# Kernel tuning notes

Hardware: AMD Instinct MI355X
Metric: run time of the kernel (lower is better)

## Reference

```python
import jax, jax.numpy as jnp
import numpy as np

BETA = 0.25  # VectorQuantizer commitment beta


def setup_inputs() -> dict:
    key = jax.random.key(0)
    k1, k2, k3, k4 = jax.random.split(key, 4)
    B, T, Zc, D, K = 8, 4096, 512, 256, 8192
    x = jax.random.normal(k1, (B, T, 1, Zc), dtype=jnp.float32)
    W = jax.random.normal(k2, (Zc, D), dtype=jnp.float32) / np.sqrt(Zc)
    b = jax.random.normal(k3, (D,), dtype=jnp.float32) * 0.01
    codebook = jax.random.normal(k4, (K, D), dtype=jnp.float32) / np.sqrt(D)
    return {"x": x, "W": W, "b": b, "codebook": codebook}


def reference(x, W, b, codebook):
    sg = jax.lax.stop_gradient
    # quant_conv: Linear(z_channels -> embed_dim) after squeezing dim 2
    h = jnp.einsum('btc,cd->btd', jnp.squeeze(x, 2), W) + b  # [B,T,D]
    B, T, D = h.shape
    flat = h.reshape(-1, D)  # [B*T, D]
    # squared L2 distances to codebook: ||z||^2 + ||e||^2 - 2 z.e
    d = (jnp.sum(flat * flat, axis=1, keepdims=True)
         + jnp.sum(codebook * codebook, axis=1)
         - 2.0 * flat @ codebook.T)  # [B*T, K]
    idx = jnp.argmin(d, axis=1)  # [B*T]
    zq = jnp.take(codebook, idx, axis=0).reshape(B, T, D)
    # codebook + commitment loss
    emb_loss = (BETA * jnp.mean((sg(zq) - h) ** 2)
                + jnp.mean((zq - sg(h)) ** 2))
    # straight-through estimator
    zq = h + sg(zq - h)
    quant = zq[..., None]  # [B,T,D,1], matching h.unsqueeze(-1) layout
    return quant, emb_loss
```

## Files before the change

kernel.cpp:

```cpp
#include <hip/hip_runtime.h>
#include <stdint.h>

#define M_TOT 32768
#define ZC 512
#define DD 256
#define KCODES 8192
#define NGRAN 512
#define MARGIN 0.15f
#define NBUCKET 256

typedef _Float16 half8   __attribute__((ext_vector_type(8)));
typedef _Float16 half2v  __attribute__((ext_vector_type(2)));
typedef float    float4v __attribute__((ext_vector_type(4)));
typedef float    float16v __attribute__((ext_vector_type(16)));

#define OFF_H     0ull
#define OFF_HT    33554432ull
#define OFF_CBT   50331648ull
#define OFF_HH    54525952ull
#define OFF_EE    54657024ull
#define OFF_LOSSP 54689792ull
#define OFF_SMIN  54691840ull
#define OFF_WTH   OFF_SMIN
#define OFF_WTL   (OFF_SMIN + 524288ull)

#define ASYNC_CP16(gp, lp)                                                     \
  __builtin_amdgcn_global_load_lds(                                            \
      (const __attribute__((address_space(1))) void*)(gp),                     \
      (__attribute__((address_space(3))) void*)(lp), 16, 0, 0)

__global__ __launch_bounds__(256) void k_prep_w(const float* __restrict__ W,
                                                _Float16* __restrict__ wt_hi,
                                                _Float16* __restrict__ wt_lo) {
    const int idx = blockIdx.x * 256 + threadIdx.x;
    const int n = idx & 255, k = idx >> 8;
    const float v = W[(size_t)k * DD + n];
    const _Float16 hi = (_Float16)v;
    const _Float16 lo = (_Float16)(v - (float)hi);
    const int off = (((n >> 5) * 64 + (k >> 3)) << 8) + ((n & 31) << 3) + (k & 7);
    wt_hi[off] = hi;
    wt_lo[off] = lo;
}

__global__ __launch_bounds__(256) void k_gemm1(const float* __restrict__ x,
                                               const _Float16* __restrict__ wt_hi,
                                               const _Float16* __restrict__ wt_lo,
                                               const float* __restrict__ b,
                                               float* __restrict__ h) {
    __shared__ _Float16 sH[64 * 64];
    __shared__ _Float16 sL[64 * 64];
    const int tid = threadIdx.x, lane = tid & 63, w = tid >> 6;
    const int wy = w >> 1, wx = w & 1;
    const int m0 = blockIdx.x * 64;

    float16v acc[4];
#pragma unroll
    for (int j = 0; j < 4; ++j) acc[j] = (float16v)(0.0f);

    for (int kb = 0; kb < ZC; kb += 64) {
        __syncthreads();
        {
            const int m = tid & 63;
            const int kp = tid >> 6;
#pragma unroll
            for (int i2 = 0; i2 < 2; ++i2) {
                const int kg = kp * 2 + i2;
                const float* src = x + (size_t)(m0 + m) * ZC + kb + kg * 8;
                float4v v0 = *(const float4v*)src;
                float4v v1 = *(const float4v*)(src + 4);
                half8 hi, lo;
                float vv[8] = {v0.x, v0.y, v0.z, v0.w, v1.x, v1.y, v1.z, v1.w};
#pragma unroll
                for (int j = 0; j < 8; ++j) {
                    hi[j] = (_Float16)vv[j];
                    lo[j] = (_Float16)(vv[j] - (float)hi[j]);
                }
                const int off = (((m >> 5) * 8 + kg) << 8) + ((m & 31) << 3);
                *(half8*)&sH[off] = hi;
                *(half8*)&sL[off] = lo;
            }
        }
        __syncthreads();
#pragma unroll
        for (int s = 0; s < 4; ++s) {
            const int S = (kb >> 4) + s;
            half8 ah = *(const half8*)&sH[((wy * 8 + 2 * s) << 8) + lane * 8];
            half8 al = *(const half8*)&sL[((wy * 8 + 2 * s) << 8) + lane * 8];
#pragma unroll
            for (int nf = 0; nf < 4; ++nf) {
                const int nblk = wx * 4 + nf;
                const size_t boff = ((size_t)(nblk * 64 + 2 * S) << 8) + lane * 8;
                half8 bh = *(const half8*)&wt_hi[boff];
                half8 bl = *(const half8*)&wt_lo[boff];
                acc[nf] = __builtin_amdgcn_mfma_f32_32x32x16_f16(ah, bh, acc[nf], 0, 0, 0);
                acc[nf] = __builtin_amdgcn_mfma_f32_32x32x16_f16(ah, bl, acc[nf], 0, 0, 0);
                acc[nf] = __builtin_amdgcn_mfma_f32_32x32x16_f16(al, bh, acc[nf], 0, 0, 0);
            }
        }
    }
#pragma unroll
    for (int nf = 0; nf < 4; ++nf) {
        const int col = wx * 128 + nf * 32 + (lane & 31);
        const float bias = b[col];
#pragma unroll
        for (int r = 0; r < 16; ++r) {
            const int row = m0 + wy * 32 + (r & 3) + 8 * (r >> 2) + 4 * (lane >> 5);
            h[(size_t)row * DD + col] = acc[nf][r] + bias;
        }
    }
}

__global__ __launch_bounds__(256) void k_prep_h(const float* __restrict__ h,
                                                _Float16* __restrict__ ht,
                                                float* __restrict__ hh) {
    const int lane = threadIdx.x & 63, w = threadIdx.x >> 6;
    const int row = blockIdx.x * 4 + w;
    float4v v = *(const float4v*)&h[(size_t)row * DD + lane * 4];
    half2v p0, p1;
    p0.x = (_Float16)v.x; p0.y = (_Float16)v.y;
    p1.x = (_Float16)v.z; p1.y = (_Float16)v.w;
    const size_t off = ((size_t)((row >> 5) * 32 + (lane >> 1)) << 8) +
                       ((row & 31) << 3) + ((lane & 1) << 2);
    *(half2v*)&ht[off] = p0;
    *(half2v*)&ht[off + 2] = p1;
    float s = v.x * v.x + v.y * v.y + v.z * v.z + v.w * v.w;
#pragma unroll
    for (int o = 32; o; o >>= 1) s += __shfl_down(s, o);
    if (lane == 0) hh[row] = s;
}

__global__ __launch_bounds__(256) void k_prep_cb(const float* __restrict__ cb,
                                                 _Float16* __restrict__ cbt,
                                                 float* __restrict__ ee,
                                                 float* __restrict__ loss_part) {
    if (blockIdx.x == 0) loss_part[threadIdx.x] = 0.0f;
    const int lane = threadIdx.x & 63, w = threadIdx.x >> 6;
    const int code = blockIdx.x * 4 + w;
    float4v v = *(const float4v*)&cb[(size_t)code * DD + lane * 4];
    half2v p0, p1;
    p0.x = (_Float16)v.x; p0.y = (_Float16)v.y;
    p1.x = (_Float16)v.z; p1.y = (_Float16)v.w;
    const size_t off = ((size_t)((code >> 5) * 32 + (lane >> 1)) << 8) +
                       ((code & 31) << 3) + ((lane & 1) << 2);
    *(half2v*)&cbt[off] = p0;
    *(half2v*)&cbt[off + 2] = p1;
    float s = v.x * v.x + v.y * v.y + v.z * v.z + v.w * v.w;
#pragma unroll
    for (int o = 32; o; o >>= 1) s += __shfl_down(s, o);
    if (lane == 0) ee[code] = s;
}

__global__ __launch_bounds__(256, 2) void k_dist(const _Float16* __restrict__ ht,
                                                 const _Float16* __restrict__ cbt,
                                                 const float* __restrict__ ee,
                                                 _Float16* __restrict__ smin) {
    __shared__ _Float16 sB[2][64 * 256];
    const int tid = threadIdx.x, lane = tid & 63, w = tid >> 6;
    const int lw = lane & 31, csel = lane >> 5;
    const int bx = blockIdx.x;
    const int by = blockIdx.y;

    half8 afr[2][16];
    const size_t lo = (size_t)lane * 8;
#pragma unroll
    for (int mi = 0; mi < 2; ++mi) {
        const _Float16* base = cbt + (size_t)(bx * 8 + w * 2 + mi) * 8192;
#pragma unroll
        for (int s = 0; s < 16; ++s)
            afr[mi][s] = *(const half8*)(base + s * 512 + lo);
    }
    half8 aext[2], bext;
#pragma unroll
    for (int j = 0; j < 8; ++j) bext[j] = (_Float16)0.f;
    if (csel == 0) bext[0] = (_Float16)(-0.5f);
#pragma unroll
    for (int mi = 0; mi < 2; ++mi) {
        const float e = ee[bx * 256 + w * 64 + mi * 32 + lw];
#pragma unroll
        for (int j = 0; j < 8; ++j) aext[mi][j] = (_Float16)0.f;
        if (csel == 0) aext[mi][0] = (_Float16)e;
    }

    const _Float16* hbase = ht + (size_t)by * 1024 * 256 + (size_t)w * 4096 + lane * 8;
#define STAGE_HS(buf, t)                                                       \
    do {                                                                       \
        const _Float16* g_ = hbase + (size_t)(t) * 16384;                      \
        char* l_ = (char*)&sB[(buf)][0] + w * 8192;                            \
        _Pragma("unroll")                                                      \
        for (int i_ = 0; i_ < 8; ++i_)                                         \
            ASYNC_CP16(g_ + i_ * 512, l_ + i_ * 1024);                         \
    } while (0)

#define LDB(sb_, nj_, s_)                                                      \
    (*(const half8*)&(sb_)[(size_t)((((nj_) * 32) + 2 * (s_) + csel) << 8) + lw * 8])

#define EPI(accA, accB, nj_)                                                   \
    do {                                                                       \
        float g0a = (accA)[0], g1a = (accA)[8];                                \
        float g0b = (accB)[0], g1b = (accB)[8];                                \
        _Pragma("unroll")                                                      \
        for (int r = 1; r < 8; ++r) {                                          \
            g0a = fmaxf(g0a, (accA)[r]);  g1a = fmaxf(g1a, (accA)[8 + r]);     \
            g0b = fmaxf(g0b, (accB)[r]);  g1b = fmaxf(g1b, (accB)[8 + r]);     \
        }                                                                      \
        g0a = fmaxf(g0a, __shfl_xor(g0a, 32));                                 \
        g1a = fmaxf(g1a, __shfl_xor(g1a, 32));                                 \
        g0b = fmaxf(g0b, __shfl_xor(g0b, 32));                                 \
        g1b = fmaxf(g1b, __shfl_xor(g1b, 32));                                 \
        if (lane < 32) {                                                       \
            const int row_ = r0_ + (nj_) * 32 + lane;                          \
            const int gb_ = bx * 16 + w * 4;                                   \
            smin[(size_t)(gb_ + 0) * M_TOT + row_] = (_Float16)(-2.f * g0a);   \
            smin[(size_t)(gb_ + 1) * M_TOT + row_] = (_Float16)(-2.f * g1a);   \
            smin[(size_t)(gb_ + 2) * M_TOT + row_] = (_Float16)(-2.f * g0b);   \
            smin[(size_t)(gb_ + 3) * M_TOT + row_] = (_Float16)(-2.f * g1b);   \
        }                                                                      \
    } while (0)

#define COMPUTE_HS(buf, t)                                                     \
    do {                                                                       \
        const int r0_ = by * 1024 + (t) * 64;                                  \
        const _Float16* sb_ = &sB[(buf)][0];                                   \
        float16v A00 = (float16v)(0.f), A01 = (float16v)(0.f);                 \
        float16v A10 = (float16v)(0.f), A11 = (float16v)(0.f);                 \
        __builtin_amdgcn_s_setprio(1);                                         \
        _Pragma("unroll")                                                      \
        for (int s = 0; s < 16; ++s) {                                         \
            half8 bf0 = LDB(sb_, 0, s);                                        \
            half8 bf1 = LDB(sb_, 1, s);                                        \
            A00 = __builtin_amdgcn_mfma_f32_32x32x16_f16(afr[0][s], bf0, A00, 0, 0, 0); \
            A01 = __builtin_amdgcn_mfma_f32_32x32x16_f16(afr[1][s], bf0, A01, 0, 0, 0); \
            A10 = __builtin_amdgcn_mfma_f32_32x32x16_f16(afr[0][s], bf1, A10, 0, 0, 0); \
            A11 = __builtin_amdgcn_mfma_f32_32x32x16_f16(afr[1][s], bf1, A11, 0, 0, 0); \
        }                                                                      \
        A00 = __builtin_amdgcn_mfma_f32_32x32x16_f16(aext[0], bext, A00, 0, 0, 0); \
        A01 = __builtin_amdgcn_mfma_f32_32x32x16_f16(aext[1], bext, A01, 0, 0, 0); \
        A10 = __builtin_amdgcn_mfma_f32_32x32x16_f16(aext[0], bext, A10, 0, 0, 0); \
        A11 = __builtin_amdgcn_mfma_f32_32x32x16_f16(aext[1], bext, A11, 0, 0, 0); \
        __builtin_amdgcn_s_setprio(0);                                         \
        EPI(A00, A01, 0);                                                      \
        EPI(A10, A11, 1);                                                      \
    } while (0)

    STAGE_HS(0, 0);
    STAGE_HS(1, 1);
    asm volatile("s_waitcnt vmcnt(8)" ::: "memory");
    __builtin_amdgcn_s_barrier();
    __builtin_amdgcn_sched_barrier(0);
    COMPUTE_HS(0, 0);
    __builtin_amdgcn_sched_barrier(0);
    __builtin_amdgcn_s_barrier();

#pragma unroll 1
    for (int t = 1; t < 15; ++t) {
        const int cur = t & 1;
        STAGE_HS(cur ^ 1, t + 1);
        asm volatile("s_waitcnt vmcnt(16)" ::: "memory");
        __builtin_amdgcn_s_barrier();
        __builtin_amdgcn_sched_barrier(0);
        COMPUTE_HS(cur, t);
        __builtin_amdgcn_sched_barrier(0);
        __builtin_amdgcn_s_barrier();
    }
    asm volatile("s_waitcnt vmcnt(8)" ::: "memory");
    __builtin_amdgcn_s_barrier();
    __builtin_amdgcn_sched_barrier(0);
    COMPUTE_HS(1, 15);

#undef STAGE_HS
#undef COMPUTE_HS
#undef LDB
#undef EPI
}

__global__ __launch_bounds__(256, 2) void k_select(const float* __restrict__ h,
                                                   const float* __restrict__ cb,
                                                   const float* __restrict__ hh,
                                                   const float* __restrict__ ee,
                                                   const _Float16* __restrict__ smin,
                                                   float* __restrict__ out,
                                                   float* __restrict__ loss_part) {
    __shared__ _Float16 sS[64][512];
    const int t = threadIdx.x, lane = t & 63, w = t >> 6;
    const int r0 = blockIdx.x * 64;

    for (int gi = t; gi < NGRAN; gi += 256) {
        const _Float16* src = smin + (size_t)gi * M_TOT + r0;
#pragma unroll
        for (int c = 0; c < 8; ++c) {
            half8 v = *(const half8*)(src + c * 8);
#pragma unroll
            for (int j = 0; j < 8; ++j) sS[c * 8 + j][gi] = v[j];
        }
    }
    __syncthreads();

    float lossacc = 0.0f;
    for (int i = 0; i < 16; ++i) {
        const int row = r0 + w * 16 + i;
        float4v hv = *(const float4v*)&h[(size_t)row * DD + lane * 4];
        half8 sm = *(const half8*)&sS[w * 16 + i][lane * 8];
        float vmin = 1e30f;
        float sv[8];
#pragma unroll
        for (int j = 0; j < 8; ++j) {
            sv[j] = (float)sm[j];
            vmin = fminf(vmin, sv[j]);
        }
        float m2 = vmin;
#pragma unroll
        for (int o = 32; o; o >>= 1) m2 = fminf(m2, __shfl_xor(m2, o));
        const float thr = m2 + MARGIN;
        unsigned flags = 0;
#pragma unroll
        for (int j = 0; j < 8; ++j)
            if (sv[j] <= thr) flags |= (1u << j);

        unsigned long long act = __ballot(flags != 0);
        unsigned long long bestk = ~0ull;
        const float hhv = hh[row];
        while (act) {
            const int ln = __ffsll((long long)act) - 1;
            act &= act - 1;
            unsigned fl = (unsigned)__shfl((int)flags, ln);
            while (fl) {
                const int j = __ffs(fl) - 1;
                fl &= fl - 1;
                const int g = ln * 8 + j;
#pragma unroll
                for (int c = 0; c < 16; ++c) {
                    const int code = g * 16 + c;
                    float4v cv = *(const float4v*)&cb[(size_t)code * DD + lane * 4];
                    float s = hv.x * cv.x + hv.y * cv.y + hv.z * cv.z + hv.w * cv.w;
#pragma unroll
                    for (int o = 32; o; o >>= 1) s += __shfl_xor(s, o);
                    const float d = (hhv + ee[code]) - 2.0f * s;
                    const unsigned bts = __float_as_uint(d);
                    const unsigned mb =
                        bts ^ (unsigned)(((int)bts >> 31) | 0x80000000);
                    const unsigned long long key =
                        ((unsigned long long)mb << 32) | (unsigned)code;
                    if (key < bestk) bestk = key;
                }
            }
        }
        const unsigned best = (unsigned)(bestk & 0xffffffffull);
        float4v cv = *(const float4v*)&cb[(size_t)best * DD + lane * 4];
        *(float4v*)&out[(size_t)row * DD + lane * 4] = cv;
        const float dx = cv.x - hv.x, dy = cv.y - hv.y;
        const float dz = cv.z - hv.z, dw = cv.w - hv.w;
        lossacc += dx * dx + dy * dy + dz * dz + dw * dw;
    }
#pragma unroll
    for (int o = 32; o; o >>= 1) lossacc += __shfl_xor(lossacc, o);
    if (lane == 0)
        atomicAdd(&loss_part[(blockIdx.x * 4 + w) & (NBUCKET - 1)], lossacc);
}

__global__ __launch_bounds__(256) void k_final(const float* __restrict__ loss_part,
                                               float* __restrict__ out) {
    const int t = threadIdx.x;
    float s = loss_part[t];
#pragma unroll
    for (int off = 32; off; off >>= 1) s += __shfl_down(s, off);
    __shared__ float wsum[4];
    if ((t & 63) == 0) wsum[t >> 6] = s;
    __syncthreads();
    if (t == 0)
        out[0] = 1.25f * ((wsum[0] + wsum[1]) + (wsum[2] + wsum[3]))
                 / (float)(M_TOT * DD);
}

extern "C" void kernel_launch(void* const* d_in, const int* in_sizes, int n_in,
                              void* d_out, int out_size, void* d_ws, size_t ws_size,
                              hipStream_t stream) {
    const float* x  = (const float*)d_in[0];
    const float* W  = (const float*)d_in[1];
    const float* b  = (const float*)d_in[2];
    const float* cb = (const float*)d_in[3];
    float* out = (float*)d_out;

    char* ws = (char*)d_ws;
    float* h        = (float*)(ws + OFF_H);
    _Float16* ht    = (_Float16*)(ws + OFF_HT);
    _Float16* cbt   = (_Float16*)(ws + OFF_CBT);
    _Float16* wt_hi = (_Float16*)(ws + OFF_WTH);
    _Float16* wt_lo = (_Float16*)(ws + OFF_WTL);
    float* hh       = (float*)(ws + OFF_HH);
    float* ee       = (float*)(ws + OFF_EE);
    _Float16* smin  = (_Float16*)(ws + OFF_SMIN);
    float* loss_part = (float*)(ws + OFF_LOSSP);

    hipLaunchKernelGGL(k_prep_w, dim3(512), dim3(256), 0, stream, W, wt_hi, wt_lo);
    hipLaunchKernelGGL(k_prep_cb, dim3(KCODES / 4), dim3(256), 0, stream,
                       cb, cbt, ee, loss_part);
    hipLaunchKernelGGL(k_gemm1, dim3(M_TOT / 64), dim3(256), 0, stream,
                       x, wt_hi, wt_lo, b, h);
    hipLaunchKernelGGL(k_prep_h, dim3(M_TOT / 4), dim3(256), 0, stream,
                       h, ht, hh);
    hipLaunchKernelGGL(k_dist, dim3(KCODES / 256, M_TOT / 1024), dim3(256),
                       0, stream, ht, cbt, ee, smin);
    hipLaunchKernelGGL(k_select, dim3(M_TOT / 64), dim3(256), 0, stream,
                       h, cb, hh, ee, smin, out, loss_part);
    hipLaunchKernelGGL(k_final, dim3(1), dim3(256), 0, stream,
                       loss_part, out + (size_t)M_TOT * DD);
}
```

Baseline: 367.2 us.

## Fuse h fp16 transpose and norms into GEMM1 epilogue, merge prep kernels

Merges the W-split and codebook prep kernels into one launch. Moves the fp16 tiled conversion of h and its squared row norms into the GEMM1 epilogue, staged through a swizzled LDS tile, so the separate k_prep_h pass that re-read h from global memory is gone. This saves one full read of h (32 MB) and two kernel launches. In exchange GEMM1 uses 32 KB more LDS and gains extra barriers, which may lower its occupancy.

```diff
diff --git a/kernel.cpp b/kernel.cpp
--- a/kernel.cpp
+++ b/kernel.cpp
@@ -29,27 +29,55 @@
       (const __attribute__((address_space(1))) void*)(gp),                     \
       (__attribute__((address_space(3))) void*)(lp), 16, 0, 0)
 
-__global__ __launch_bounds__(256) void k_prep_w(const float* __restrict__ W,
-                                                _Float16* __restrict__ wt_hi,
-                                                _Float16* __restrict__ wt_lo) {
-    const int idx = blockIdx.x * 256 + threadIdx.x;
-    const int n = idx & 255, k = idx >> 8;
-    const float v = W[(size_t)k * DD + n];
-    const _Float16 hi = (_Float16)v;
-    const _Float16 lo = (_Float16)(v - (float)hi);
-    const int off = (((n >> 5) * 64 + (k >> 3)) << 8) + ((n & 31) << 3) + (k & 7);
-    wt_hi[off] = hi;
-    wt_lo[off] = lo;
+__global__ __launch_bounds__(256) void k_prep(const float* __restrict__ W,
+                                              const float* __restrict__ cb,
+                                              _Float16* __restrict__ wt_hi,
+                                              _Float16* __restrict__ wt_lo,
+                                              _Float16* __restrict__ cbt,
+                                              float* __restrict__ ee,
+                                              float* __restrict__ loss_part) {
+    const int bx = blockIdx.x;
+    if (bx < 512) {
+        const int idx = bx * 256 + threadIdx.x;
+        const int n = idx & 255, k = idx >> 8;
+        const float v = W[(size_t)k * DD + n];
+        const _Float16 hi = (_Float16)v;
+        const _Float16 lo = (_Float16)(v - (float)hi);
+        const int off = (((n >> 5) * 64 + (k >> 3)) << 8) + ((n & 31) << 3) + (k & 7);
+        wt_hi[off] = hi;
+        wt_lo[off] = lo;
+        return;
+    }
+    if (bx == 512) loss_part[threadIdx.x] = 0.0f;
+    const int lane = threadIdx.x & 63, w = threadIdx.x >> 6;
+    const int code = (bx - 512) * 4 + w;
+    float4v v = *(const float4v*)&cb[(size_t)code * DD + lane * 4];
+    half2v p0, p1;
+    p0.x = (_Float16)v.x; p0.y = (_Float16)v.y;
+    p1.x = (_Float16)v.z; p1.y = (_Float16)v.w;
+    const size_t off = ((size_t)((code >> 5) * 32 + (lane >> 1)) << 8) +
+                       ((code & 31) << 3) + ((lane & 1) << 2);
+    *(half2v*)&cbt[off] = p0;
+    *(half2v*)&cbt[off + 2] = p1;
+    float s = v.x * v.x + v.y * v.y + v.z * v.z + v.w * v.w;
+#pragma unroll
+    for (int o = 32; o; o >>= 1) s += __shfl_down(s, o);
+    if (lane == 0) ee[code] = s;
 }
 
 __global__ __launch_bounds__(256) void k_gemm1(const float* __restrict__ x,
                                                const _Float16* __restrict__ wt_hi,
                                                const _Float16* __restrict__ wt_lo,
                                                const float* __restrict__ b,
-                                               float* __restrict__ h) {
+                                               float* __restrict__ h,
+                                               _Float16* __restrict__ ht,
+                                               float* __restrict__ hh) {
     __shared__ _Float16 sH[64 * 64];
     __shared__ _Float16 sL[64 * 64];
+    __shared__ _Float16 sT[64 * 256];
+    __shared__ float sHH[64];
     const int tid = threadIdx.x, lane = tid & 63, w = tid >> 6;
+    const int lw = lane & 31, csel = lane >> 5;
     const int wy = w >> 1, wx = w & 1;
     const int m0 = blockIdx.x * 64;
 
@@ -98,56 +126,47 @@
             }
         }
     }
-#pragma unroll
-    for (int nf = 0; nf < 4; ++nf) {
-        const int col = wx * 128 + nf * 32 + (lane & 31);
-        const float bias = b[col];
+    float bias[4];
+#pragma unroll
+    for (int nf = 0; nf < 4; ++nf) bias[nf] = b[wx * 128 + nf * 32 + lw];
+
+    float pr[16];
+    __syncthreads();
+#pragma unroll
+    for (int r = 0; r < 16; ++r) {
+        const int row = wy * 32 + (r & 3) + 8 * (r >> 2) + 4 * csel;
+        float p = 0.f;
+#pragma unroll
+        for (int nf = 0; nf < 4; ++nf) {
+            const int col = wx * 128 + nf * 32 + lw;
+            const float v = acc[nf][r] + bias[nf];
+            h[(size_t)(m0 + row) * DD + col] = v;
+            sT[row * 256 + (col ^ ((row & 7) << 3))] = (_Float16)v;
+            p += v * v;
+        }
+#pragma unroll
+        for (int o = 16; o; o >>= 1) p += __shfl_xor(p, o);
+        pr[r] = p;
+        if (wx == 0 && lw == 0) sHH[row] = p;
+    }
+    __syncthreads();
+    if (wx == 1 && lw == 0) {
 #pragma unroll
         for (int r = 0; r < 16; ++r) {
-            const int row = m0 + wy * 32 + (r & 3) + 8 * (r >> 2) + 4 * (lane >> 5);
-            h[(size_t)row * DD + col] = acc[nf][r] + bias;
-        }
-    }
-}
-
-__global__ __launch_bounds__(256) void k_prep_h(const float* __restrict__ h,
-                                                _Float16* __restrict__ ht,
-                                                float* __restrict__ hh) {
-    const int lane = threadIdx.x & 63, w = threadIdx.x >> 6;
-    const int row = blockIdx.x * 4 + w;
-    float4v v = *(const float4v*)&h[(size_t)row * DD + lane * 4];
-    half2v p0, p1;
-    p0.x = (_Float16)v.x; p0.y = (_Float16)v.y;
-    p1.x = (_Float16)v.z; p1.y = (_Float16)v.w;
-    const size_t off = ((size_t)((row >> 5) * 32 + (lane >> 1)) << 8) +
-                       ((row & 31) << 3) + ((lane & 1) << 2);
-    *(half2v*)&ht[off] = p0;
-    *(half2v*)&ht[off + 2] = p1;
-    float s = v.x * v.x + v.y * v.y + v.z * v.z + v.w * v.w;
-#pragma unroll
-    for (int o = 32; o; o >>= 1) s += __shfl_down(s, o);
-    if (lane == 0) hh[row] = s;
-}
-
-__global__ __launch_bounds__(256) void k_prep_cb(const float* __restrict__ cb,
-                                                 _Float16* __restrict__ cbt,
-                                                 float* __restrict__ ee,
-                                                 float* __restrict__ loss_part) {
-    if (blockIdx.x == 0) loss_part[threadIdx.x] = 0.0f;
-    const int lane = threadIdx.x & 63, w = threadIdx.x >> 6;
-    const int code = blockIdx.x * 4 + w;
-    float4v v = *(const float4v*)&cb[(size_t)code * DD + lane * 4];
-    half2v p0, p1;
-    p0.x = (_Float16)v.x; p0.y = (_Float16)v.y;
-    p1.x = (_Float16)v.z; p1.y = (_Float16)v.w;
-    const size_t off = ((size_t)((code >> 5) * 32 + (lane >> 1)) << 8) +
-                       ((code & 31) << 3) + ((lane & 1) << 2);
-    *(half2v*)&cbt[off] = p0;
-    *(half2v*)&cbt[off + 2] = p1;
-    float s = v.x * v.x + v.y * v.y + v.z * v.z + v.w * v.w;
-#pragma unroll
-    for (int o = 32; o; o >>= 1) s += __shfl_down(s, o);
-    if (lane == 0) ee[code] = s;
+            const int row = wy * 32 + (r & 3) + 8 * (r >> 2) + 4 * csel;
+            sHH[row] += pr[r];
+        }
+    }
+    __syncthreads();
+#pragma unroll
+    for (int i = 0; i < 8; ++i) {
+        const int j = tid + i * 256;
+        const int c = j >> 5, rr = j & 31;
+        const int row = (c >> 5) * 32 + rr, kg = c & 31;
+        half8 v = *(const half8*)&sT[row * 256 + ((kg * 8) ^ ((row & 7) << 3))];
+        *(half8*)&ht[(size_t)m0 * 256 + (size_t)j * 8] = v;
+    }
+    if (tid < 64) hh[m0 + tid] = sHH[tid];
 }
 
 __global__ __launch_bounds__(256, 2) void k_dist(const _Float16* __restrict__ ht,
@@ -391,13 +410,10 @@
     _Float16* smin  = (_Float16*)(ws + OFF_SMIN);
     float* loss_part = (float*)(ws + OFF_LOSSP);
 
-    hipLaunchKernelGGL(k_prep_w, dim3(512), dim3(256), 0, stream, W, wt_hi, wt_lo);
-    hipLaunchKernelGGL(k_prep_cb, dim3(KCODES / 4), dim3(256), 0, stream,
-                       cb, cbt, ee, loss_part);
+    hipLaunchKernelGGL(k_prep, dim3(512 + KCODES / 4), dim3(256), 0, stream,
+                       W, cb, wt_hi, wt_lo, cbt, ee, loss_part);
     hipLaunchKernelGGL(k_gemm1, dim3(M_TOT / 64), dim3(256), 0, stream,
-                       x, wt_hi, wt_lo, b, h);
-    hipLaunchKernelGGL(k_prep_h, dim3(M_TOT / 4), dim3(256), 0, stream,
-                       h, ht, hh);
+                       x, wt_hi, wt_lo, b, h, ht, hh);
     hipLaunchKernelGGL(k_dist, dim3(KCODES / 256, M_TOT / 1024), dim3(256),
                        0, stream, ht, cbt, ee, smin);
     hipLaunchKernelGGL(k_select, dim3(M_TOT / 64), dim3(256), 0, stream,
```

Result: faster. 354.4 us (-3.5%).
